# Kernel optimization log

Measured on AMD Instinct MI355X. Metric: run time of the kernel, lower is better.

## Reference

```python
import jax, jax.numpy as jnp
import numpy as np
from jax import lax

D = 8          # conv_out_size
HID = 128      # lstm hidden
EMB = 32       # word embed
GD = 256       # g/f mlp width


def _coords():
    # faithful to cvt_coord with python3 float division on first component
    c = np.zeros((D * D, 2), dtype=np.float32)
    for i in range(D * D):
        c[i, 0] = (i / D - D / 2) / (D / 2.0)
        c[i, 1] = (i % D - D / 2) / (D / 2.0)
    return jnp.asarray(c)


def _conv_bn(x, k, b, gamma, beta):
    y = lax.conv_general_dilated(x, k, (2, 2), [(1, 1), (1, 1)],
                                 dimension_numbers=('NCHW', 'OIHW', 'NCHW'))
    y = jax.nn.relu(y + b[None, :, None, None])
    m = y.mean((0, 2, 3))
    v = ((y - m[None, :, None, None]) ** 2).mean((0, 2, 3))  # biased var (train-mode BN)
    y = (y - m[None, :, None, None]) * lax.rsqrt(v + 1e-5)[None, :, None, None]
    return gamma[None, :, None, None] * y + beta[None, :, None, None]


def setup_inputs() -> dict:
    key = jax.random.key(0)
    ks = iter(jax.random.split(key, 48))
    B, T, QV, AV = 64, 18, 90, 28
    n = lambda sh, s=0.1: jax.random.normal(next(ks), sh, jnp.float32) * s
    inp = {
        'img': jax.random.normal(next(ks), (B, 3, 128, 128), jnp.float32),
        'qst_idxs': jax.random.randint(next(ks), (B, T), 0, QV),
        'emb': n((QV, EMB)).at[0].set(0.0),  # padding_idx=0
        'W_ih': n((4 * HID, EMB)), 'W_hh': n((4 * HID, HID)),
        'b_ih': n((4 * HID,)), 'b_hh': n((4 * HID,)),
        'k1': n((24, 3, 3, 3)), 'cb1': n((24,)), 'g1': jnp.ones((24,)), 'be1': jnp.zeros((24,)),
        'k2': n((24, 24, 3, 3)), 'cb2': n((24,)), 'g2': jnp.ones((24,)), 'be2': jnp.zeros((24,)),
        'k3': n((24, 24, 3, 3)), 'cb3': n((24,)), 'g3': jnp.ones((24,)), 'be3': jnp.zeros((24,)),
        'k4': n((24, 24, 3, 3)), 'cb4': n((24,)), 'g4': jnp.ones((24,)), 'be4': jnp.zeros((24,)),
        'Wg1': n((GD, 180)), 'bg1': n((GD,)),
        'Wg2': n((GD, GD)), 'bg2': n((GD,)),
        'Wg3': n((GD, GD)), 'bg3': n((GD,)),
        'Wg4': n((GD, GD)), 'bg4': n((GD,)),
        'Wf1': n((GD, GD)), 'bf1': n((GD,)),
        'Wf2': n((GD, GD)), 'bf2': n((GD,)),
        'Wf3': n((AV, GD)), 'bf3': n((AV,)),
        'h0': jax.random.normal(next(ks), (B, HID), jnp.float32),
        'c0': jax.random.normal(next(ks), (B, HID), jnp.float32),
    }
    return inp


def reference(img, qst_idxs, emb, W_ih, W_hh, b_ih, b_hh,
              k1, cb1, g1, be1, k2, cb2, g2, be2, k3, cb3, g3, be3, k4, cb4, g4, be4,
              Wg1, bg1, Wg2, bg2, Wg3, bg3, Wg4, bg4,
              Wf1, bf1, Wf2, bf2, Wf3, bf3, h0, c0):
    B = img.shape[0]
    # --- question encoder: embedding (padding_idx=0) + LSTM, take final CELL state ---
    we = emb[qst_idxs] * (qst_idxs != 0)[..., None].astype(emb.dtype)  # [B,T,32]

    def step(carry, x_t):
        h, c = carry
        gates = x_t @ W_ih.T + h @ W_hh.T + (b_ih + b_hh)
        i, f, g, o = jnp.split(gates, 4, axis=-1)
        c = jax.nn.sigmoid(f) * c + jax.nn.sigmoid(i) * jnp.tanh(g)
        h = jax.nn.sigmoid(o) * jnp.tanh(c)
        return (h, c), None

    (h_n, c_n), _ = lax.scan(step, (h0, c0), we.transpose(1, 0, 2))
    qst = c_n  # original uses self.hidden[1][-1] == cell state, [B,128]

    # --- conv stack ---
    x = _conv_bn(img, k1, cb1, g1, be1)
    x = _conv_bn(x, k2, cb2, g2, be2)
    x = _conv_bn(x, k3, cb3, g3, be3)
    x = _conv_bn(x, k4, cb4, g4, be4)  # [B,24,8,8]

    xf = x.reshape(B, 24, D * D).transpose(0, 2, 1)            # [B,64,24]
    xf = jnp.concatenate([xf, jnp.broadcast_to(_coords(), (B, D * D, 2))], 2)  # [B,64,26]

    # --- g-MLP over all pairs; first linear decomposed across x_i / x_j / qst ---
    # pair (k,j) feature = [x_flat[j](26), x_flat[k](26), qst(128)]
    Ai = xf @ Wg1[:, :26].T                    # [B,64,256], x_i part (index j)
    Aj = xf @ Wg1[:, 26:52].T                  # [B,64,256], x_j part (index k)
    Q = qst @ Wg1[:, 52:].T + bg1              # [B,256]
    h = jax.nn.relu(Ai[:, None, :, :] + Aj[:, :, None, :] + Q[:, None, None, :])  # [B,64,64,256]
    h = jax.nn.relu(h @ Wg2.T + bg2)
    h = jax.nn.relu(h @ Wg3.T + bg3)
    h = jax.nn.relu(h @ Wg4.T + bg4)
    xg = h.sum((1, 2))                          # [B,256] sum-pool over pairs

    # --- f-MLP (dropout = identity in eval) ---
    xfc = jax.nn.relu(xg @ Wf1.T + bf1)
    xfc = jax.nn.relu(xfc @ Wf2.T + bf2)
    logits = xfc @ Wf3.T + bf3
    return jax.nn.log_softmax(logits, axis=-1)
```

## Files before the change

### kernel.cpp

```cpp
#include <hip/hip_runtime.h>
#include <math.h>

typedef __bf16 bf16x8 __attribute__((ext_vector_type(8)));
typedef float  f32x4  __attribute__((ext_vector_type(4)));
typedef float  f32x16 __attribute__((ext_vector_type(16)));

#define DEVFN __device__ __forceinline__

DEVFN unsigned short f2bf(float f) {
    union { float f; unsigned u; } v; v.f = f;
    unsigned r = v.u + 0x7FFFu + ((v.u >> 16) & 1u);
    return (unsigned short)(r >> 16);
}
DEVFN float sigmoidf_(float x) { return 1.0f / (1.0f + expf(-x)); }

__global__ void lstm_kernel(const int* __restrict__ qidx, const float* __restrict__ emb,
                            const float* __restrict__ Wih, const float* __restrict__ Whh,
                            const float* __restrict__ bih, const float* __restrict__ bhh,
                            const float* __restrict__ h0, const float* __restrict__ c0,
                            float* __restrict__ qst)
{
    int b = blockIdx.x, tid = threadIdx.x;
    __shared__ float hs[128], cs[128], xs[32], gs[512];
    if (tid < 128) { hs[tid] = h0[b*128 + tid]; cs[tid] = c0[b*128 + tid]; }
    float bsum = bih[tid] + bhh[tid];
    for (int t = 0; t < 18; ++t) {
        if (tid < 32) {
            int id = qidx[b*18 + t];
            xs[tid] = (id != 0) ? emb[id*32 + tid] : 0.0f;
        }
        __syncthreads();
        float g = bsum;
        const float* wi = Wih + tid*32;
        #pragma unroll
        for (int d = 0; d < 32; ++d) g += xs[d] * wi[d];
        const float* wh = Whh + tid*128;
        for (int d = 0; d < 128; ++d) g += hs[d] * wh[d];
        gs[tid] = g;
        __syncthreads();
        if (tid < 128) {
            float ig = sigmoidf_(gs[tid]);
            float fg = sigmoidf_(gs[128 + tid]);
            float gg = tanhf(gs[256 + tid]);
            float og = sigmoidf_(gs[384 + tid]);
            float cn = fg * cs[tid] + ig * gg;
            cs[tid] = cn;
            hs[tid] = og * tanhf(cn);
        }
        __syncthreads();
    }
    if (tid < 128) qst[b*128 + tid] = cs[tid];
}

__launch_bounds__(256, 2)
__global__ void conv1_kernel(const float* __restrict__ img, const float* __restrict__ wk,
                             const float* __restrict__ cb, float* __restrict__ y1)
{
    __shared__ float simg[3][33][128];
    __shared__ float wl[3][9][24];
    __shared__ float cbs[24];
    int b = blockIdx.x, t = blockIdx.y, tid = threadIdx.x;
    for (int i = tid; i < 648; i += 256) {
        int co = i / 27, rem = i % 27;
        int ci = rem / 9, tap = rem % 9;
        wl[ci][tap][co] = wk[i];
    }
    if (tid < 24) cbs[tid] = cb[tid];
    int base = 32*t - 1;
    for (int i = tid; i < 3*33*128; i += 256) {
        int ci = i / (33*128); int r2 = i % (33*128);
        int row = r2 / 128, colx = r2 % 128;
        int ih = base + row;
        simg[ci][row][colx] = (ih >= 0 && ih < 128) ?
            img[((size_t)(b*3 + ci)*128 + ih)*128 + colx] : 0.f;
    }
    __syncthreads();

    int ow = tid & 63;
    int os0 = tid >> 6;
    float acc[4][24];
    #pragma unroll
    for (int r = 0; r < 4; ++r)
        #pragma unroll
        for (int c = 0; c < 24; ++c) acc[r][c] = 0.f;

    #pragma unroll
    for (int ci = 0; ci < 3; ++ci)
      #pragma unroll
      for (int kh = 0; kh < 3; ++kh)
        #pragma unroll
        for (int kw = 0; kw < 3; ++kw) {
            int iw = ow*2 + kw - 1;
            bool v = (iw >= 0 && iw < 128);
            float x[4];
            #pragma unroll
            for (int r = 0; r < 4; ++r) {
                int os = os0 + 4*r;
                x[r] = v ? simg[ci][2*os + kh][iw] : 0.f;
            }
            const float* wv = &wl[ci][kh*3 + kw][0];
            #pragma unroll
            for (int c4 = 0; c4 < 6; ++c4) {
                float4 w4 = *reinterpret_cast<const float4*>(wv + c4*4);
                #pragma unroll
                for (int r = 0; r < 4; ++r) {
                    acc[r][c4*4+0] += x[r]*w4.x;
                    acc[r][c4*4+1] += x[r]*w4.y;
                    acc[r][c4*4+2] += x[r]*w4.z;
                    acc[r][c4*4+3] += x[r]*w4.w;
                }
            }
        }

    #pragma unroll
    for (int co = 0; co < 24; ++co) {
        float bb = cbs[co];
        #pragma unroll
        for (int r = 0; r < 4; ++r) {
            int oh = t*16 + os0 + 4*r;
            y1[((size_t)(b*24 + co)*64 + oh)*64 + ow] = fmaxf(acc[r][co] + bb, 0.f);
        }
    }
}

__launch_bounds__(128, 4)
__global__ void conv2_kernel(const float* __restrict__ y1, const float* __restrict__ wk,
                             const float* __restrict__ cb, const float* __restrict__ ab,
                             float* __restrict__ y2)
{
    __shared__ float sin2[24][5][64];
    __shared__ float wl[24][9][24];
    __shared__ float cbs[24];
    int b = blockIdx.x, t = blockIdx.y, tid = threadIdx.x;
    for (int i = tid; i < 5184; i += 128) {
        int co = i / 216, rem = i % 216;
        int ci = rem / 9, tap = rem % 9;
        wl[ci][tap][co] = wk[i];
    }
    if (tid < 24) cbs[tid] = cb[tid];
    int base = 4*t - 1;
    for (int i = tid; i < 24*5*64; i += 128) {
        int ci = i / (5*64); int r2 = i % (5*64);
        int row = r2 / 64, colx = r2 % 64;
        int ih = base + row;
        sin2[ci][row][colx] = (ih >= 0 && ih < 64) ?
            y1[((size_t)(b*24 + ci)*64 + ih)*64 + colx] * ab[ci] + ab[24 + ci] : 0.f;
    }
    __syncthreads();

    int pos = tid & 63;
    int ow = pos & 31, os = pos >> 5;
    int ch = tid >> 6;
    int oh = 2*t + os;
    float acc[12];
    #pragma unroll
    for (int c = 0; c < 12; ++c) acc[c] = 0.f;

    for (int ci = 0; ci < 24; ++ci) {
        #pragma unroll
        for (int kh = 0; kh < 3; ++kh)
          #pragma unroll
          for (int kw = 0; kw < 3; ++kw) {
            int iw = ow*2 + kw - 1;
            float x = (iw >= 0 && iw < 64) ? sin2[ci][2*os + kh][iw] : 0.f;
            const float* wv = &wl[ci][kh*3 + kw][ch*12];
            #pragma unroll
            for (int c4 = 0; c4 < 3; ++c4) {
                float4 w4 = *reinterpret_cast<const float4*>(wv + c4*4);
                acc[c4*4+0] += x*w4.x;
                acc[c4*4+1] += x*w4.y;
                acc[c4*4+2] += x*w4.z;
                acc[c4*4+3] += x*w4.w;
            }
          }
    }
    #pragma unroll
    for (int c = 0; c < 12; ++c) {
        int co = ch*12 + c;
        y2[((size_t)(b*24 + co)*32 + oh)*32 + ow] = fmaxf(acc[c] + cbs[co], 0.f);
    }
}

__launch_bounds__(256, 2)
__global__ void conv_kernel(const float* __restrict__ in, const float* __restrict__ wk,
                            const float* __restrict__ cb, const float* __restrict__ ab,
                            float* __restrict__ out,
                            int Cin, int Hin, int Win, int Hout, int Wout)
{
    int cob = blockIdx.x;
    int co = cob % 24, b = cob / 24;
    int tid = threadIdx.x;
    __shared__ float sw[24*9];
    __shared__ float so9[9];
    __shared__ float bias;
    if (tid < Cin*9) {
        int ci = tid / 9, t = tid % 9;
        float a_ = ab ? ab[ci] : 1.0f;
        sw[tid] = wk[(co*Cin + ci)*9 + t] * a_;
    }
    if (tid < 9) {
        float s = 0.f;
        if (ab) {
            for (int ci = 0; ci < Cin; ++ci)
                s += ab[Cin + ci] * wk[(co*Cin + ci)*9 + tid];
        }
        so9[tid] = s;
    }
    if (tid == 0) bias = cb[co];
    __syncthreads();

    int HW = Hout * Wout;
    int pos = blockIdx.y * 256 + tid;
    if (pos >= HW) return;
    int ow = pos % Wout, oh = pos / Wout;

    float acc = bias;
    #pragma unroll
    for (int kh = 0; kh < 3; ++kh) {
        int ih = oh*2 + kh - 1;
        bool vh = (ih >= 0 && ih < Hin);
        #pragma unroll
        for (int kw = 0; kw < 3; ++kw) {
            int iw = ow*2 + kw - 1;
            if (vh && iw >= 0 && iw < Win) acc += so9[kh*3 + kw];
        }
    }
    const float* ipb = in + ((size_t)b * Cin) * Hin * Win;
    for (int ci = 0; ci < Cin; ++ci) {
        const float* ip = ipb + (size_t)ci * Hin * Win;
        const float* swp = sw + ci*9;
        #pragma unroll
        for (int kh = 0; kh < 3; ++kh) {
            int ih = oh*2 + kh - 1;
            if (ih < 0 || ih >= Hin) continue;
            #pragma unroll
            for (int kw = 0; kw < 3; ++kw) {
                int iw = ow*2 + kw - 1;
                if (iw < 0 || iw >= Win) continue;
                acc += ip[ih*Win + iw] * swp[kh*3 + kw];
            }
        }
    }
    out[((size_t)(b*24 + co)) * HW + pos] = fmaxf(acc, 0.0f);
}

__global__ void bn_partial_kernel(const float* __restrict__ y, float* __restrict__ part,
                                  int HW, int nb)
{
    int c = blockIdx.x;
    int s = blockIdx.y;
    int S = gridDim.y;
    int tid = threadIdx.x;
    int n4 = HW >> 2;
    float sum = 0.f, sum2 = 0.f;
    for (int b = s * nb; b < (s + 1) * nb; ++b) {
        const float4* p = reinterpret_cast<const float4*>(y + ((size_t)(b*24 + c)) * HW);
        for (int i = tid; i < n4; i += 256) {
            float4 v = p[i];
            sum  += v.x + v.y + v.z + v.w;
            sum2 += v.x*v.x + v.y*v.y + v.z*v.z + v.w*v.w;
        }
    }
    __shared__ float rs[256], rs2[256];
    rs[tid] = sum; rs2[tid] = sum2;
    __syncthreads();
    for (int st = 128; st > 0; st >>= 1) {
        if (tid < st) { rs[tid] += rs[tid + st]; rs2[tid] += rs2[tid + st]; }
        __syncthreads();
    }
    if (tid == 0) {
        part[(c * S + s) * 2]     = rs[0];
        part[(c * S + s) * 2 + 1] = rs2[0];
    }
}

__global__ void bn_final_kernel(const float* __restrict__ part, const float* __restrict__ gamma,
                                const float* __restrict__ beta, float* __restrict__ ab,
                                int S, int N)
{
    int c = threadIdx.x;
    if (c >= 24) return;
    float s = 0.f, s2 = 0.f;
    for (int i = 0; i < S; ++i) { s += part[(c*S + i)*2]; s2 += part[(c*S + i)*2 + 1]; }
    float m = s / N;
    float v = s2 / N - m * m;
    float r = rsqrtf(v + 1e-5f);
    float a = gamma[c] * r;
    ab[c] = a; ab[24 + c] = beta[c] - m * a;
}

__global__ void aiajq_kernel(const float* __restrict__ y4, const float* __restrict__ ab4,
                             const float* __restrict__ qst,
                             const float* __restrict__ Wg1, const float* __restrict__ bg1,
                             float* __restrict__ Ai, float* __restrict__ Aj, float* __restrict__ Q)
{
    int b = blockIdx.x, c = threadIdx.x;
    __shared__ float xfl[64 * 26];
    __shared__ float qv[128];
    for (int i = c; i < 64*24; i += 256) {
        int p = i / 24, ch = i % 24;
        xfl[p*26 + ch] = y4[((size_t)(b*24 + ch)) * 64 + p] * ab4[ch] + ab4[24 + ch];
    }
    if (c < 64) {
        xfl[c*26 + 24] = ((float)c / 8.0f - 4.0f) * 0.25f;
        xfl[c*26 + 25] = ((float)(c % 8) - 4.0f) * 0.25f;
    }
    if (c < 128) qv[c] = qst[b*128 + c];
    __syncthreads();
    const float* w = Wg1 + (size_t)c * 180;
    float wa[26], wb[26];
    #pragma unroll
    for (int d = 0; d < 26; ++d) { wa[d] = w[d]; wb[d] = w[26 + d]; }
    float q = bg1[c];
    for (int d = 0; d < 128; ++d) q += qv[d] * w[52 + d];
    Q[b*256 + c] = q;
    for (int j = 0; j < 64; ++j) {
        const float* xr = xfl + j*26;
        float sa = 0.f, sb = 0.f;
        #pragma unroll
        for (int d = 0; d < 26; ++d) { sa += xr[d]*wa[d]; sb += xr[d]*wb[d]; }
        Ai[((size_t)(b*64 + j))*256 + c] = sa;
        Aj[((size_t)(b*64 + j))*256 + c] = sb;
    }
}

__global__ void cvt_w_kernel(const float* __restrict__ Wg2, const float* __restrict__ Wg3,
                             const float* __restrict__ Wg4,
                             unsigned short* __restrict__ Wt2, unsigned short* __restrict__ Wt3,
                             unsigned short* __restrict__ Wt4)
{
    int i = blockIdx.x * 256 + threadIdx.x;
    int seg = i >> 16, idx = i & 65535;
    const float* src = (seg == 0) ? Wg2 : (seg == 1) ? Wg3 : Wg4;
    unsigned short* dst = (seg == 0) ? Wt2 : (seg == 1) ? Wt3 : Wt4;
    int col = idx >> 8, k = idx & 255;
    dst[(k >> 3)*2048 + col*8 + (k & 7)] = f2bf(src[idx]);
}

__launch_bounds__(512, 4)
__global__ void gmlp_kernel(const float* __restrict__ Ai, const float* __restrict__ Aj,
                            const float* __restrict__ Q,
                            const unsigned short* __restrict__ Wt2, const float* __restrict__ bg2,
                            const unsigned short* __restrict__ Wt3, const float* __restrict__ bg3,
                            const unsigned short* __restrict__ Wt4, const float* __restrict__ bg4,
                            float* __restrict__ partial)
{
    constexpr int LDP = 264;
    __shared__ __align__(16) unsigned short buf[128 * LDP];
    int tid = threadIdx.x;
    int blk = blockIdx.x;
    int b = blk >> 5;
    int k0 = (blk & 31) << 1;

    {
        int c = tid & 255, g = tid >> 8;
        float ajq = Aj[((size_t)(b*64 + k0 + g))*256 + c] + Q[b*256 + c];
        const float* aip = Ai + ((size_t)b*64)*256 + c;
        unsigned short* bp = buf + (g*64)*LDP + c;
        #pragma unroll 4
        for (int j = 0; j < 64; ++j) {
            float v = aip[(size_t)j*256] + ajq;
            bp[j*LDP] = f2bf(fmaxf(v, 0.f));
        }
    }
    __syncthreads();

    int l = tid & 63, w = tid >> 6;
    int lid = l & 31, hi = l >> 5;
    int col = w*32 + lid;

    const unsigned short* Ws[3] = {Wt2, Wt3, Wt4};
    const float* Bs[3] = {bg2, bg3, bg4};

    #pragma unroll
    for (int layer = 0; layer < 3; ++layer) {
        const unsigned short* W = Ws[layer];
        float bc = Bs[layer][col];
        f32x16 acc[4];
        #pragma unroll
        for (int rg = 0; rg < 4; ++rg)
            #pragma unroll
            for (int i = 0; i < 16; ++i) acc[rg][i] = 0.f;

        const unsigned short* wp = W + (size_t)hi*2048 + col*8;
        const unsigned short* ap = buf + lid*LDP + hi*8;

        #pragma unroll
        for (int kk = 0; kk < 16; ++kk) {
            bf16x8 bF = *reinterpret_cast<const bf16x8*>(wp + kk*4096);
            #pragma unroll
            for (int rg = 0; rg < 4; ++rg) {
                bf16x8 aF = *reinterpret_cast<const bf16x8*>(ap + rg*32*LDP + kk*16);
                acc[rg] = __builtin_amdgcn_mfma_f32_32x32x16_bf16(aF, bF, acc[rg], 0, 0, 0);
            }
        }

        if (layer < 2) {
            __syncthreads();
            #pragma unroll
            for (int rg = 0; rg < 4; ++rg)
                #pragma unroll
                for (int reg = 0; reg < 16; ++reg) {
                    int row = rg*32 + (reg & 3) + 8*(reg >> 2) + 4*hi;
                    buf[row*LDP + col] = f2bf(fmaxf(acc[rg][reg] + bc, 0.f));
                }
            __syncthreads();
        } else {
            float cs = 0.f;
            #pragma unroll
            for (int rg = 0; rg < 4; ++rg)
                #pragma unroll
                for (int reg = 0; reg < 16; ++reg)
                    cs += fmaxf(acc[rg][reg] + bc, 0.f);
            cs += __shfl_xor(cs, 32);
            if (hi == 0)
                partial[(size_t)blk*256 + col] = cs;
        }
    }
}

__global__ void fmlp_kernel(const float* __restrict__ partial,
                            const float* __restrict__ Wf1, const float* __restrict__ bf1,
                            const float* __restrict__ Wf2, const float* __restrict__ bf2,
                            const float* __restrict__ Wf3, const float* __restrict__ bf3,
                            float* __restrict__ out)
{
    int b = blockIdx.x, tid = threadIdx.x;
    __shared__ float v0[256], v1[256], lgt[28];
    {
        float s0 = 0.f, s1 = 0.f, s2 = 0.f, s3 = 0.f;
        const float* p = partial + ((size_t)b * 32) * 256 + tid;
        #pragma unroll
        for (int k = 0; k < 32; k += 4) {
            s0 += p[(size_t)(k+0) * 256];
            s1 += p[(size_t)(k+1) * 256];
            s2 += p[(size_t)(k+2) * 256];
            s3 += p[(size_t)(k+3) * 256];
        }
        v0[tid] = (s0 + s1) + (s2 + s3);
    }
    __syncthreads();
    {
        float s = bf1[tid];
        const float4* wr = reinterpret_cast<const float4*>(Wf1 + (size_t)tid * 256);
        for (int k4 = 0; k4 < 64; ++k4) {
            float4 wv = wr[k4];
            s += wv.x*v0[k4*4+0] + wv.y*v0[k4*4+1] + wv.z*v0[k4*4+2] + wv.w*v0[k4*4+3];
        }
        v1[tid] = fmaxf(s, 0.f);
    }
    __syncthreads();
    {
        float s = bf2[tid];
        const float4* wr = reinterpret_cast<const float4*>(Wf2 + (size_t)tid * 256);
        for (int k4 = 0; k4 < 64; ++k4) {
            float4 wv = wr[k4];
            s += wv.x*v1[k4*4+0] + wv.y*v1[k4*4+1] + wv.z*v1[k4*4+2] + wv.w*v1[k4*4+3];
        }
        v0[tid] = fmaxf(s, 0.f);
    }
    __syncthreads();
    if (tid < 28) {
        float s = bf3[tid];
        const float4* wr = reinterpret_cast<const float4*>(Wf3 + (size_t)tid * 256);
        for (int k4 = 0; k4 < 64; ++k4) {
            float4 wv = wr[k4];
            s += wv.x*v0[k4*4+0] + wv.y*v0[k4*4+1] + wv.z*v0[k4*4+2] + wv.w*v0[k4*4+3];
        }
        lgt[tid] = s;
    }
    __syncthreads();
    if (tid == 0) {
        float mx = -1e30f;
        for (int i = 0; i < 28; ++i) mx = fmaxf(mx, lgt[i]);
        float se = 0.f;
        for (int i = 0; i < 28; ++i) se += expf(lgt[i] - mx);
        float lse = mx + logf(se);
        for (int i = 0; i < 28; ++i) out[b*28 + i] = lgt[i] - lse;
    }
}

extern "C" void kernel_launch(void* const* d_in, const int* in_sizes, int n_in,
                              void* d_out, int out_size, void* d_ws, size_t ws_size,
                              hipStream_t stream)
{
    (void)in_sizes; (void)n_in; (void)out_size; (void)ws_size;
    const float* img = (const float*)d_in[0];
    const int*   qidx= (const int*)  d_in[1];
    const float* emb = (const float*)d_in[2];
    const float* Wih = (const float*)d_in[3];
    const float* Whh = (const float*)d_in[4];
    const float* bih = (const float*)d_in[5];
    const float* bhh = (const float*)d_in[6];
    const float* k1  = (const float*)d_in[7];  const float* cb1=(const float*)d_in[8];
    const float* g1  = (const float*)d_in[9];  const float* be1=(const float*)d_in[10];
    const float* k2  = (const float*)d_in[11]; const float* cb2=(const float*)d_in[12];
    const float* g2  = (const float*)d_in[13]; const float* be2=(const float*)d_in[14];
    const float* k3  = (const float*)d_in[15]; const float* cb3=(const float*)d_in[16];
    const float* g3  = (const float*)d_in[17]; const float* be3=(const float*)d_in[18];
    const float* k4  = (const float*)d_in[19]; const float* cb4=(const float*)d_in[20];
    const float* g4  = (const float*)d_in[21]; const float* be4=(const float*)d_in[22];
    const float* Wg1 = (const float*)d_in[23]; const float* bg1=(const float*)d_in[24];
    const float* Wg2 = (const float*)d_in[25]; const float* bg2=(const float*)d_in[26];
    const float* Wg3 = (const float*)d_in[27]; const float* bg3=(const float*)d_in[28];
    const float* Wg4 = (const float*)d_in[29]; const float* bg4=(const float*)d_in[30];
    const float* Wf1 = (const float*)d_in[31]; const float* bf1=(const float*)d_in[32];
    const float* Wf2 = (const float*)d_in[33]; const float* bf2=(const float*)d_in[34];
    const float* Wf3 = (const float*)d_in[35]; const float* bf3=(const float*)d_in[36];
    const float* h0  = (const float*)d_in[37]; const float* c0 =(const float*)d_in[38];
    float* out = (float*)d_out;

    float* ws = (float*)d_ws;
    float* y1 = ws;   ws += 64*24*64*64;
    float* y2 = ws;   ws += 64*24*32*32;
    float* y3 = ws;   ws += 64*24*16*16;
    float* y4 = ws;   ws += 64*24*8*8;
    float* ab1 = ws;  ws += 48;
    float* ab2 = ws;  ws += 48;
    float* ab3 = ws;  ws += 48;
    float* ab4 = ws;  ws += 48;
    float* bnp = ws;  ws += 24*16*2;
    float* qst = ws;  ws += 64*128;
    float* Ai  = ws;  ws += 64*64*256;
    float* Aj  = ws;  ws += 64*64*256;
    float* Qb  = ws;  ws += 64*256;
    unsigned short* Wt2 = (unsigned short*)ws; ws += 65536/2;
    unsigned short* Wt3 = (unsigned short*)ws; ws += 65536/2;
    unsigned short* Wt4 = (unsigned short*)ws; ws += 65536/2;
    float* partial = ws; ws += 2048*256;

    lstm_kernel<<<64, 512, 0, stream>>>(qidx, emb, Wih, Whh, bih, bhh, h0, c0, qst);

    conv1_kernel<<<dim3(64, 4), 256, 0, stream>>>(img, k1, cb1, y1);
    bn_partial_kernel<<<dim3(24,16), 256, 0, stream>>>(y1, bnp, 64*64, 4);
    bn_final_kernel<<<1, 32, 0, stream>>>(bnp, g1, be1, ab1, 16, 64*64*64);
    conv2_kernel<<<dim3(64, 16), 128, 0, stream>>>(y1, k2, cb2, ab1, y2);
    bn_partial_kernel<<<dim3(24,8), 256, 0, stream>>>(y2, bnp, 32*32, 8);
    bn_final_kernel<<<1, 32, 0, stream>>>(bnp, g2, be2, ab2, 8, 64*32*32);
    conv_kernel<<<dim3(64*24, 1), 256, 0, stream>>>(y2, k3, cb3, ab2, y3, 24, 32, 32, 16, 16);
    bn_partial_kernel<<<dim3(24,4), 256, 0, stream>>>(y3, bnp, 16*16, 16);
    bn_final_kernel<<<1, 32, 0, stream>>>(bnp, g3, be3, ab3, 4, 64*16*16);
    conv_kernel<<<dim3(64*24, 1), 256, 0, stream>>>(y3, k4, cb4, ab3, y4, 24, 16, 16, 8, 8);
    bn_partial_kernel<<<dim3(24,1), 256, 0, stream>>>(y4, bnp, 8*8, 64);
    bn_final_kernel<<<1, 32, 0, stream>>>(bnp, g4, be4, ab4, 1, 64*8*8);

    aiajq_kernel<<<64, 256, 0, stream>>>(y4, ab4, qst, Wg1, bg1, Ai, Aj, Qb);
    cvt_w_kernel<<<768, 256, 0, stream>>>(Wg2, Wg3, Wg4, Wt2, Wt3, Wt4);

    gmlp_kernel<<<2048, 512, 0, stream>>>(Ai, Aj, Qb, Wt2, bg2, Wt3, bg3, Wt4, bg4, partial);
    fmlp_kernel<<<64, 256, 0, stream>>>(partial, Wf1, bf1, Wf2, bf2, Wf3, bf3, out);
}
```

Measured before the change: 535.3 us.

## Fuse BN finalize into consumers, merge weight cvt into LSTM, retile g-MLP MFMA

Removes the four bn_final launches by recomputing the per-channel BN scale and offset inside each consuming kernel (conv2, conv_kernel, aiajq). Folds the bf16 weight conversion into extra blocks of the LSTM launch. Retiles the g-MLP so each wave computes a 2x2 block of 32x32 MFMA tiles, reusing A and B fragments, and vectorises the first-layer build with float2 loads and packed bf16 stores. Partials double to two per block, so fmlp sums 64 per batch. The cost is redundant BN folding in every block.

```diff
diff --git a/kernel.cpp b/kernel.cpp
--- a/kernel.cpp
+++ b/kernel.cpp
@@ -2,7 +2,6 @@
 #include <math.h>
 
 typedef __bf16 bf16x8 __attribute__((ext_vector_type(8)));
-typedef float  f32x4  __attribute__((ext_vector_type(4)));
 typedef float  f32x16 __attribute__((ext_vector_type(16)));
 
 #define DEVFN __device__ __forceinline__
@@ -14,13 +13,27 @@
 }
 DEVFN float sigmoidf_(float x) { return 1.0f / (1.0f + expf(-x)); }
 
-__global__ void lstm_kernel(const int* __restrict__ qidx, const float* __restrict__ emb,
-                            const float* __restrict__ Wih, const float* __restrict__ Whh,
-                            const float* __restrict__ bih, const float* __restrict__ bhh,
-                            const float* __restrict__ h0, const float* __restrict__ c0,
-                            float* __restrict__ qst)
-{
-    int b = blockIdx.x, tid = threadIdx.x;
+__global__ void lstm_cvt_kernel(const int* __restrict__ qidx, const float* __restrict__ emb,
+                                const float* __restrict__ Wih, const float* __restrict__ Whh,
+                                const float* __restrict__ bih, const float* __restrict__ bhh,
+                                const float* __restrict__ h0, const float* __restrict__ c0,
+                                float* __restrict__ qst,
+                                const float* __restrict__ Wg2, const float* __restrict__ Wg3,
+                                const float* __restrict__ Wg4,
+                                unsigned short* __restrict__ Wt2, unsigned short* __restrict__ Wt3,
+                                unsigned short* __restrict__ Wt4)
+{
+    int tid = threadIdx.x;
+    if (blockIdx.x >= 64) {
+        int i = (blockIdx.x - 64) * 512 + tid;
+        int seg = i >> 16, idx = i & 65535;
+        const float* src = (seg == 0) ? Wg2 : (seg == 1) ? Wg3 : Wg4;
+        unsigned short* dst = (seg == 0) ? Wt2 : (seg == 1) ? Wt3 : Wt4;
+        int col = idx >> 8, k = idx & 255;
+        dst[(k >> 3)*2048 + col*8 + (k & 7)] = f2bf(src[idx]);
+        return;
+    }
+    int b = blockIdx.x;
     __shared__ float hs[128], cs[128], xs[32], gs[512];
     if (tid < 128) { hs[tid] = h0[b*128 + tid]; cs[tid] = c0[b*128 + tid]; }
     float bsum = bih[tid] + bhh[tid];
@@ -123,28 +136,77 @@
     }
 }
 
+__global__ void bn_partial_kernel(const float* __restrict__ y, float* __restrict__ part,
+                                  int HW, int nb)
+{
+    int c = blockIdx.x;
+    int s = blockIdx.y;
+    int S = gridDim.y;
+    int tid = threadIdx.x;
+    int n4 = HW >> 2;
+    float sum = 0.f, sum2 = 0.f;
+    for (int b = s * nb; b < (s + 1) * nb; ++b) {
+        const float4* p = reinterpret_cast<const float4*>(y + ((size_t)(b*24 + c)) * HW);
+        for (int i = tid; i < n4; i += 256) {
+            float4 v = p[i];
+            sum  += v.x + v.y + v.z + v.w;
+            sum2 += v.x*v.x + v.y*v.y + v.z*v.z + v.w*v.w;
+        }
+    }
+    __shared__ float rs[256], rs2[256];
+    rs[tid] = sum; rs2[tid] = sum2;
+    __syncthreads();
+    for (int st = 128; st > 0; st >>= 1) {
+        if (tid < st) { rs[tid] += rs[tid + st]; rs2[tid] += rs2[tid + st]; }
+        __syncthreads();
+    }
+    if (tid == 0) {
+        part[(c * S + s) * 2]     = rs[0];
+        part[(c * S + s) * 2 + 1] = rs2[0];
+    }
+}
+
+#define BN_FOLD(bnp, gamma, beta, S, N, abs_, abo_, tid)                    \
+    if (tid < 24) {                                                          \
+        float s_ = 0.f, s2_ = 0.f;                                           \
+        for (int i_ = 0; i_ < (S); ++i_) {                                   \
+            s_  += (bnp)[((tid)*(S) + i_)*2];                                \
+            s2_ += (bnp)[((tid)*(S) + i_)*2 + 1];                            \
+        }                                                                    \
+        float m_ = s_ / (N);                                                 \
+        float v_ = s2_ / (N) - m_*m_;                                        \
+        float r_ = rsqrtf(v_ + 1e-5f);                                       \
+        float a_ = (gamma)[tid] * r_;                                        \
+        (abs_)[tid] = a_; (abo_)[tid] = (beta)[tid] - m_*a_;                 \
+    }
+
 __launch_bounds__(128, 4)
 __global__ void conv2_kernel(const float* __restrict__ y1, const float* __restrict__ wk,
-                             const float* __restrict__ cb, const float* __restrict__ ab,
+                             const float* __restrict__ cb,
+                             const float* __restrict__ bnp, const float* __restrict__ gamma,
+                             const float* __restrict__ beta,
                              float* __restrict__ y2)
 {
     __shared__ float sin2[24][5][64];
     __shared__ float wl[24][9][24];
     __shared__ float cbs[24];
+    __shared__ float abs_[24], abo_[24];
     int b = blockIdx.x, t = blockIdx.y, tid = threadIdx.x;
+    BN_FOLD(bnp, gamma, beta, 16, 262144, abs_, abo_, tid);
     for (int i = tid; i < 5184; i += 128) {
         int co = i / 216, rem = i % 216;
         int ci = rem / 9, tap = rem % 9;
         wl[ci][tap][co] = wk[i];
     }
     if (tid < 24) cbs[tid] = cb[tid];
+    __syncthreads();
     int base = 4*t - 1;
     for (int i = tid; i < 24*5*64; i += 128) {
         int ci = i / (5*64); int r2 = i % (5*64);
         int row = r2 / 64, colx = r2 % 64;
         int ih = base + row;
         sin2[ci][row][colx] = (ih >= 0 && ih < 64) ?
-            y1[((size_t)(b*24 + ci)*64 + ih)*64 + colx] * ab[ci] + ab[24 + ci] : 0.f;
+            y1[((size_t)(b*24 + ci)*64 + ih)*64 + colx] * abs_[ci] + abo_[ci] : 0.f;
     }
     __syncthreads();
 
@@ -183,7 +245,9 @@
 
 __launch_bounds__(256, 2)
 __global__ void conv_kernel(const float* __restrict__ in, const float* __restrict__ wk,
-                            const float* __restrict__ cb, const float* __restrict__ ab,
+                            const float* __restrict__ cb,
+                            const float* __restrict__ bnp, const float* __restrict__ gamma,
+                            const float* __restrict__ beta, int S, int N,
                             float* __restrict__ out,
                             int Cin, int Hin, int Win, int Hout, int Wout)
 {
@@ -193,24 +257,24 @@
     __shared__ float sw[24*9];
     __shared__ float so9[9];
     __shared__ float bias;
+    __shared__ float abs_[24], abo_[24];
+    BN_FOLD(bnp, gamma, beta, S, N, abs_, abo_, tid);
+    __syncthreads();
     if (tid < Cin*9) {
         int ci = tid / 9, t = tid % 9;
-        float a_ = ab ? ab[ci] : 1.0f;
-        sw[tid] = wk[(co*Cin + ci)*9 + t] * a_;
+        sw[tid] = wk[(co*Cin + ci)*9 + t] * abs_[ci];
     }
     if (tid < 9) {
         float s = 0.f;
-        if (ab) {
-            for (int ci = 0; ci < Cin; ++ci)
-                s += ab[Cin + ci] * wk[(co*Cin + ci)*9 + tid];
-        }
+        for (int ci = 0; ci < Cin; ++ci)
+            s += abo_[ci] * wk[(co*Cin + ci)*9 + tid];
         so9[tid] = s;
     }
     if (tid == 0) bias = cb[co];
     __syncthreads();
 
     int HW = Hout * Wout;
-    int pos = blockIdx.y * 256 + tid;
+    int pos = tid;
     if (pos >= HW) return;
     int ow = pos % Wout, oh = pos / Wout;
 
@@ -244,52 +308,9 @@
     out[((size_t)(b*24 + co)) * HW + pos] = fmaxf(acc, 0.0f);
 }
 
-__global__ void bn_partial_kernel(const float* __restrict__ y, float* __restrict__ part,
-                                  int HW, int nb)
-{
-    int c = blockIdx.x;
-    int s = blockIdx.y;
-    int S = gridDim.y;
-    int tid = threadIdx.x;
-    int n4 = HW >> 2;
-    float sum = 0.f, sum2 = 0.f;
-    for (int b = s * nb; b < (s + 1) * nb; ++b) {
-        const float4* p = reinterpret_cast<const float4*>(y + ((size_t)(b*24 + c)) * HW);
-        for (int i = tid; i < n4; i += 256) {
-            float4 v = p[i];
-            sum  += v.x + v.y + v.z + v.w;
-            sum2 += v.x*v.x + v.y*v.y + v.z*v.z + v.w*v.w;
-        }
-    }
-    __shared__ float rs[256], rs2[256];
-    rs[tid] = sum; rs2[tid] = sum2;
-    __syncthreads();
-    for (int st = 128; st > 0; st >>= 1) {
-        if (tid < st) { rs[tid] += rs[tid + st]; rs2[tid] += rs2[tid + st]; }
-        __syncthreads();
-    }
-    if (tid == 0) {
-        part[(c * S + s) * 2]     = rs[0];
-        part[(c * S + s) * 2 + 1] = rs2[0];
-    }
-}
-
-__global__ void bn_final_kernel(const float* __restrict__ part, const float* __restrict__ gamma,
-                                const float* __restrict__ beta, float* __restrict__ ab,
-                                int S, int N)
-{
-    int c = threadIdx.x;
-    if (c >= 24) return;
-    float s = 0.f, s2 = 0.f;
-    for (int i = 0; i < S; ++i) { s += part[(c*S + i)*2]; s2 += part[(c*S + i)*2 + 1]; }
-    float m = s / N;
-    float v = s2 / N - m * m;
-    float r = rsqrtf(v + 1e-5f);
-    float a = gamma[c] * r;
-    ab[c] = a; ab[24 + c] = beta[c] - m * a;
-}
-
-__global__ void aiajq_kernel(const float* __restrict__ y4, const float* __restrict__ ab4,
+__global__ void aiajq_kernel(const float* __restrict__ y4,
+                             const float* __restrict__ bnp, const float* __restrict__ gamma,
+                             const float* __restrict__ beta,
                              const float* __restrict__ qst,
                              const float* __restrict__ Wg1, const float* __restrict__ bg1,
                              float* __restrict__ Ai, float* __restrict__ Aj, float* __restrict__ Q)
@@ -297,9 +318,12 @@
     int b = blockIdx.x, c = threadIdx.x;
     __shared__ float xfl[64 * 26];
     __shared__ float qv[128];
+    __shared__ float abs_[24], abo_[24];
+    BN_FOLD(bnp, gamma, beta, 1, 4096, abs_, abo_, c);
+    __syncthreads();
     for (int i = c; i < 64*24; i += 256) {
         int p = i / 24, ch = i % 24;
-        xfl[p*26 + ch] = y4[((size_t)(b*24 + ch)) * 64 + p] * ab4[ch] + ab4[24 + ch];
+        xfl[p*26 + ch] = y4[((size_t)(b*24 + ch)) * 64 + p] * abs_[ch] + abo_[ch];
     }
     if (c < 64) {
         xfl[c*26 + 24] = ((float)c / 8.0f - 4.0f) * 0.25f;
@@ -324,19 +348,6 @@
     }
 }
 
-__global__ void cvt_w_kernel(const float* __restrict__ Wg2, const float* __restrict__ Wg3,
-                             const float* __restrict__ Wg4,
-                             unsigned short* __restrict__ Wt2, unsigned short* __restrict__ Wt3,
-                             unsigned short* __restrict__ Wt4)
-{
-    int i = blockIdx.x * 256 + threadIdx.x;
-    int seg = i >> 16, idx = i & 65535;
-    const float* src = (seg == 0) ? Wg2 : (seg == 1) ? Wg3 : Wg4;
-    unsigned short* dst = (seg == 0) ? Wt2 : (seg == 1) ? Wt3 : Wt4;
-    int col = idx >> 8, k = idx & 255;
-    dst[(k >> 3)*2048 + col*8 + (k & 7)] = f2bf(src[idx]);
-}
-
 __launch_bounds__(512, 4)
 __global__ void gmlp_kernel(const float* __restrict__ Ai, const float* __restrict__ Aj,
                             const float* __restrict__ Q,
@@ -353,21 +364,30 @@
     int k0 = (blk & 31) << 1;
 
     {
-        int c = tid & 255, g = tid >> 8;
-        float ajq = Aj[((size_t)(b*64 + k0 + g))*256 + c] + Q[b*256 + c];
-        const float* aip = Ai + ((size_t)b*64)*256 + c;
-        unsigned short* bp = buf + (g*64)*LDP + c;
+        int g  = tid >> 8;
+        int jh = (tid >> 7) & 1;
+        int c2 = tid & 127;
+        float2 aj = *((const float2*)(Aj + ((size_t)(b*64 + k0 + g))*256) + c2);
+        float2 qq = *((const float2*)(Q + b*256) + c2);
+        float a0 = aj.x + qq.x, a1 = aj.y + qq.y;
+        const float2* aip = (const float2*)(Ai + ((size_t)b*64)*256) + c2;
         #pragma unroll 4
-        for (int j = 0; j < 64; ++j) {
-            float v = aip[(size_t)j*256] + ajq;
-            bp[j*LDP] = f2bf(fmaxf(v, 0.f));
+        for (int j = jh*32; j < jh*32 + 32; ++j) {
+            float2 av = aip[(size_t)j*128];
+            unsigned lo = f2bf(fmaxf(av.x + a0, 0.f));
+            unsigned hv = f2bf(fmaxf(av.y + a1, 0.f));
+            *(unsigned*)(&buf[(size_t)(g*64 + j)*LDP + 2*c2]) = lo | (hv << 16);
         }
     }
     __syncthreads();
 
     int l = tid & 63, w = tid >> 6;
+    int rh = w >> 2;
+    int cg = w & 3;
     int lid = l & 31, hi = l >> 5;
-    int col = w*32 + lid;
+    int arow = rh*64 + lid;
+    int colA = cg*64 + lid;
+    int colB = colA + 32;
 
     const unsigned short* Ws[3] = {Wt2, Wt3, Wt4};
     const float* Bs[3] = {bg2, bg3, bg4};
@@ -375,46 +395,55 @@
     #pragma unroll
     for (int layer = 0; layer < 3; ++layer) {
         const unsigned short* W = Ws[layer];
-        float bc = Bs[layer][col];
-        f32x16 acc[4];
-        #pragma unroll
-        for (int rg = 0; rg < 4; ++rg)
-            #pragma unroll
-            for (int i = 0; i < 16; ++i) acc[rg][i] = 0.f;
-
-        const unsigned short* wp = W + (size_t)hi*2048 + col*8;
-        const unsigned short* ap = buf + lid*LDP + hi*8;
+        const float* bias = Bs[layer];
+        f32x16 acc00, acc01, acc10, acc11;
+        #pragma unroll
+        for (int i = 0; i < 16; ++i) { acc00[i]=0.f; acc01[i]=0.f; acc10[i]=0.f; acc11[i]=0.f; }
+
+        const unsigned short* wp0 = W + (size_t)hi*2048 + colA*8;
+        const unsigned short* wp1 = W + (size_t)hi*2048 + colB*8;
+        const unsigned short* ap  = buf + arow*LDP + hi*8;
 
         #pragma unroll
         for (int kk = 0; kk < 16; ++kk) {
-            bf16x8 bF = *reinterpret_cast<const bf16x8*>(wp + kk*4096);
-            #pragma unroll
-            for (int rg = 0; rg < 4; ++rg) {
-                bf16x8 aF = *reinterpret_cast<const bf16x8*>(ap + rg*32*LDP + kk*16);
-                acc[rg] = __builtin_amdgcn_mfma_f32_32x32x16_bf16(aF, bF, acc[rg], 0, 0, 0);
-            }
+            bf16x8 b0 = *reinterpret_cast<const bf16x8*>(wp0 + kk*4096);
+            bf16x8 b1 = *reinterpret_cast<const bf16x8*>(wp1 + kk*4096);
+            bf16x8 a0 = *reinterpret_cast<const bf16x8*>(ap + kk*16);
+            bf16x8 a1 = *reinterpret_cast<const bf16x8*>(ap + 32*LDP + kk*16);
+            acc00 = __builtin_amdgcn_mfma_f32_32x32x16_bf16(a0, b0, acc00, 0, 0, 0);
+            acc01 = __builtin_amdgcn_mfma_f32_32x32x16_bf16(a0, b1, acc01, 0, 0, 0);
+            acc10 = __builtin_amdgcn_mfma_f32_32x32x16_bf16(a1, b0, acc10, 0, 0, 0);
+            acc11 = __builtin_amdgcn_mfma_f32_32x32x16_bf16(a1, b1, acc11, 0, 0, 0);
         }
 
         if (layer < 2) {
+            float bc0 = bias[colA], bc1 = bias[colB];
             __syncthreads();
             #pragma unroll
-            for (int rg = 0; rg < 4; ++rg)
-                #pragma unroll
-                for (int reg = 0; reg < 16; ++reg) {
-                    int row = rg*32 + (reg & 3) + 8*(reg >> 2) + 4*hi;
-                    buf[row*LDP + col] = f2bf(fmaxf(acc[rg][reg] + bc, 0.f));
-                }
+            for (int reg = 0; reg < 16; ++reg) {
+                int r0 = rh*64 + (reg & 3) + 8*(reg >> 2) + 4*hi;
+                buf[r0*LDP + colA] = f2bf(fmaxf(acc00[reg] + bc0, 0.f));
+                buf[r0*LDP + colB] = f2bf(fmaxf(acc01[reg] + bc1, 0.f));
+                int r1 = r0 + 32;
+                buf[r1*LDP + colA] = f2bf(fmaxf(acc10[reg] + bc0, 0.f));
+                buf[r1*LDP + colB] = f2bf(fmaxf(acc11[reg] + bc1, 0.f));
+            }
             __syncthreads();
         } else {
-            float cs = 0.f;
+            float bc0 = bias[colA], bc1 = bias[colB];
+            float cs0 = 0.f, cs1 = 0.f;
             #pragma unroll
-            for (int rg = 0; rg < 4; ++rg)
-                #pragma unroll
-                for (int reg = 0; reg < 16; ++reg)
-                    cs += fmaxf(acc[rg][reg] + bc, 0.f);
-            cs += __shfl_xor(cs, 32);
-            if (hi == 0)
-                partial[(size_t)blk*256 + col] = cs;
+            for (int reg = 0; reg < 16; ++reg) {
+                cs0 += fmaxf(acc00[reg] + bc0, 0.f) + fmaxf(acc10[reg] + bc0, 0.f);
+                cs1 += fmaxf(acc01[reg] + bc1, 0.f) + fmaxf(acc11[reg] + bc1, 0.f);
+            }
+            cs0 += __shfl_xor(cs0, 32);
+            cs1 += __shfl_xor(cs1, 32);
+            if (hi == 0) {
+                float* pp = partial + ((size_t)blk*2 + rh)*256;
+                pp[colA] = cs0;
+                pp[colB] = cs1;
+            }
         }
     }
 }
@@ -429,9 +458,9 @@
     __shared__ float v0[256], v1[256], lgt[28];
     {
         float s0 = 0.f, s1 = 0.f, s2 = 0.f, s3 = 0.f;
-        const float* p = partial + ((size_t)b * 32) * 256 + tid;
-        #pragma unroll
-        for (int k = 0; k < 32; k += 4) {
+        const float* p = partial + ((size_t)b * 64) * 256 + tid;
+        #pragma unroll
+        for (int k = 0; k < 64; k += 4) {
             s0 += p[(size_t)(k+0) * 256];
             s1 += p[(size_t)(k+1) * 256];
             s2 += p[(size_t)(k+2) * 256];
@@ -515,10 +544,6 @@
     float* y2 = ws;   ws += 64*24*32*32;
     float* y3 = ws;   ws += 64*24*16*16;
     float* y4 = ws;   ws += 64*24*8*8;
-    float* ab1 = ws;  ws += 48;
-    float* ab2 = ws;  ws += 48;
-    float* ab3 = ws;  ws += 48;
-    float* ab4 = ws;  ws += 48;
     float* bnp = ws;  ws += 24*16*2;
     float* qst = ws;  ws += 64*128;
     float* Ai  = ws;  ws += 64*64*256;
@@ -527,25 +552,23 @@
     unsigned short* Wt2 = (unsigned short*)ws; ws += 65536/2;
     unsigned short* Wt3 = (unsigned short*)ws; ws += 65536/2;
     unsigned short* Wt4 = (unsigned short*)ws; ws += 65536/2;
-    float* partial = ws; ws += 2048*256;
-
-    lstm_kernel<<<64, 512, 0, stream>>>(qidx, emb, Wih, Whh, bih, bhh, h0, c0, qst);
+    float* partial = ws; ws += 2048*2*256;
+
+    lstm_cvt_kernel<<<448, 512, 0, stream>>>(qidx, emb, Wih, Whh, bih, bhh, h0, c0, qst,
+                                             Wg2, Wg3, Wg4, Wt2, Wt3, Wt4);
 
     conv1_kernel<<<dim3(64, 4), 256, 0, stream>>>(img, k1, cb1, y1);
     bn_partial_kernel<<<dim3(24,16), 256, 0, stream>>>(y1, bnp, 64*64, 4);
-    bn_final_kernel<<<1, 32, 0, stream>>>(bnp, g1, be1, ab1, 16, 64*64*64);
-    conv2_kernel<<<dim3(64, 16), 128, 0, stream>>>(y1, k2, cb2, ab1, y2);
+    conv2_kernel<<<dim3(64, 16), 128, 0, stream>>>(y1, k2, cb2, bnp, g1, be1, y2);
     bn_partial_kernel<<<dim3(24,8), 256, 0, stream>>>(y2, bnp, 32*32, 8);
-    bn_final_kernel<<<1, 32, 0, stream>>>(bnp, g2, be2, ab2, 8, 64*32*32);
-    conv_kernel<<<dim3(64*24, 1), 256, 0, stream>>>(y2, k3, cb3, ab2, y3, 24, 32, 32, 16, 16);
+    conv_kernel<<<dim3(64*24, 1), 256, 0, stream>>>(y2, k3, cb3, bnp, g2, be2, 8, 64*32*32,
+                                                    y3, 24, 32, 32, 16, 16);
     bn_partial_kernel<<<dim3(24,4), 256, 0, stream>>>(y3, bnp, 16*16, 16);
-    bn_final_kernel<<<1, 32, 0, stream>>>(bnp, g3, be3, ab3, 4, 64*16*16);
-    conv_kernel<<<dim3(64*24, 1), 256, 0, stream>>>(y3, k4, cb4, ab3, y4, 24, 16, 16, 8, 8);
+    conv_kernel<<<dim3(64*24, 1), 256, 0, stream>>>(y3, k4, cb4, bnp, g3, be3, 4, 64*16*16,
+                                                    y4, 24, 16, 16, 8, 8);
     bn_partial_kernel<<<dim3(24,1), 256, 0, stream>>>(y4, bnp, 8*8, 64);
-    bn_final_kernel<<<1, 32, 0, stream>>>(bnp, g4, be4, ab4, 1, 64*8*8);
-
-    aiajq_kernel<<<64, 256, 0, stream>>>(y4, ab4, qst, Wg1, bg1, Ai, Aj, Qb);
-    cvt_w_kernel<<<768, 256, 0, stream>>>(Wg2, Wg3, Wg4, Wt2, Wt3, Wt4);
+
+    aiajq_kernel<<<64, 256, 0, stream>>>(y4, bnp, g4, be4, qst, Wg1, bg1, Ai, Aj, Qb);
 
     gmlp_kernel<<<2048, 512, 0, stream>>>(Ai, Aj, Qb, Wt2, bg2, Wt3, bg3, Wt4, bg4, partial);
     fmlp_kernel<<<64, 256, 0, stream>>>(partial, Wf1, bf1, Wf2, bf2, Wf3, bf3, out);
```

Result: no change. 542.1 us (+1.3%).
